# Kernel optimization log

Measured on AMD Instinct MI355X. Metric: run time of the kernel, lower is better.

## Reference

```python
import jax, jax.numpy as jnp
import numpy as np

NODE_DIM = 512
PROMPT_DIM = 512
N_NODES = 100000
N_GRAPHS = 1024


def setup_inputs() -> dict:
    key = jax.random.key(0)
    k1, k2, k3, k4, k5, k6, k7 = jax.random.split(key, 7)
    node_feats = jax.random.normal(k1, (N_NODES, NODE_DIM), dtype=jnp.float32)
    graph_prompt = jax.random.normal(k2, (N_GRAPHS, PROMPT_DIM), dtype=jnp.float32)
    batch_idx = jnp.sort(jax.random.randint(k3, (N_NODES,), 0, N_GRAPHS))
    # Linear init ~ U(-1/sqrt(fan_in), 1/sqrt(fan_in)) like torch defaults
    fan1 = NODE_DIM + PROMPT_DIM
    b1 = 1.0 / np.sqrt(fan1)
    W1 = jax.random.uniform(k4, (fan1, NODE_DIM), minval=-b1, maxval=b1, dtype=jnp.float32)
    bias1 = jax.random.uniform(k5, (NODE_DIM,), minval=-b1, maxval=b1, dtype=jnp.float32)
    b2 = 1.0 / np.sqrt(NODE_DIM)
    W2 = jax.random.uniform(k6, (NODE_DIM, NODE_DIM), minval=-b2, maxval=b2, dtype=jnp.float32)
    bias2 = jax.random.uniform(k7, (NODE_DIM,), minval=-b2, maxval=b2, dtype=jnp.float32)
    return {"node_feats": node_feats, "graph_prompt": graph_prompt, "batch_idx": batch_idx,
            "W1": W1, "bias1": bias1, "W2": W2, "bias2": bias2}


def reference(node_feats, graph_prompt, batch_idx, W1, bias1, W2, bias2):
    # gather per-node prompt: [N, prompt_dim]
    prompt_expanded = graph_prompt[batch_idx]
    combined = jnp.concatenate([node_feats, prompt_expanded], axis=-1)  # [N, node_dim+prompt_dim]
    h = jax.nn.relu(combined @ W1 + bias1)  # [N, node_dim]
    return h @ W2 + bias2  # [N, node_dim]
```

## Files before the change

### kernel.cpp

```cpp
#include <hip/hip_runtime.h>


#define N_NODES 100000
#define MT1 782
#define NWG (MT1 * 4)

typedef __bf16 bf16x8 __attribute__((ext_vector_type(8)));
typedef float  f32x4  __attribute__((ext_vector_type(4)));
typedef unsigned short ushort_t;

__device__ __forceinline__ ushort_t f2bf(float f) {
  __bf16 b = (__bf16)f;
  return __builtin_bit_cast(unsigned short, b);
}

__device__ __forceinline__ bf16x8 cvt8(const float* p) {
  float4 x = *(const float4*)p;
  float4 y = *(const float4*)(p + 4);
  bf16x8 v;
  v[0] = (__bf16)x.x; v[1] = (__bf16)x.y; v[2] = (__bf16)x.z; v[3] = (__bf16)x.w;
  v[4] = (__bf16)y.x; v[5] = (__bf16)y.y; v[6] = (__bf16)y.z; v[7] = (__bf16)y.w;
  return v;
}

__device__ __forceinline__ bf16x8 cvt8v(float4 x, float4 y) {
  bf16x8 v;
  v[0] = (__bf16)x.x; v[1] = (__bf16)x.y; v[2] = (__bf16)x.z; v[3] = (__bf16)x.w;
  v[4] = (__bf16)y.x; v[5] = (__bf16)y.y; v[6] = (__bf16)y.z; v[7] = (__bf16)y.w;
  return v;
}

__device__ __forceinline__ void gload_lds16(const void* g, void* l) {
  __builtin_amdgcn_global_load_lds(
      (const __attribute__((address_space(1))) void*)g,
      (__attribute__((address_space(3))) void*)l, 16, 0, 0);
}

__global__ void prep_kernel(const float* __restrict__ W1, const float* __restrict__ W2,
                            ushort_t* __restrict__ W1T, ushort_t* __restrict__ W2T) {
  int i = blockIdx.x * 256 + threadIdx.x;
  if (i < 524288) {
    int n = i >> 10, k = i & 1023;
    W1T[i] = f2bf(W1[k * 512 + n]);
  } else if (i < 786432) {
    int j = i - 524288;
    int n = j >> 9, k = j & 511;
    W2T[j] = f2bf(W2[k * 512 + n]);
  }
}

__global__ __launch_bounds__(256, 4) void p2_kernel(
    const float* __restrict__ gp, const ushort_t* __restrict__ W1T,
    const float* __restrict__ bias1, float* __restrict__ P2) {
  const int tid = threadIdx.x, lane = tid & 63, wid = tid >> 6;
  const int lc = lane & 15, lr = lane >> 4;
  const int m0 = (blockIdx.x >> 1) * 32;
  const int col0 = (blockIdx.x & 1) * 256 + wid * 64;

  f32x4 acc[2][4];
#pragma unroll
  for (int i = 0; i < 2; ++i)
#pragma unroll
    for (int j = 0; j < 4; ++j) acc[i][j] = {0.f, 0.f, 0.f, 0.f};

  const float* a0 = gp + (size_t)(m0 + lc) * 512;
  const ushort_t* bb = W1T + (size_t)(col0 + lc) * 1024 + 512;

#pragma unroll 2
  for (int kt = 0; kt < 8; ++kt) {
    bf16x8 bfr[2][4];
#pragma unroll
    for (int kk = 0; kk < 2; ++kk)
#pragma unroll
      for (int j = 0; j < 4; ++j)
        bfr[kk][j] = *(const bf16x8*)(bb + (size_t)j * 16 * 1024 + kt * 64 + kk * 32 + lr * 8);
    bf16x8 af[2][2];
#pragma unroll
    for (int i = 0; i < 2; ++i)
#pragma unroll
      for (int kk = 0; kk < 2; ++kk)
        af[i][kk] = cvt8(a0 + (size_t)i * 16 * 512 + kt * 64 + kk * 32 + lr * 8);
#pragma unroll
    for (int kk = 0; kk < 2; ++kk)
#pragma unroll
      for (int i = 0; i < 2; ++i)
#pragma unroll
        for (int j = 0; j < 4; ++j)
          acc[i][j] = __builtin_amdgcn_mfma_f32_16x16x32_bf16(af[i][kk], bfr[kk][j], acc[i][j], 0, 0, 0);
  }

#pragma unroll
  for (int i = 0; i < 2; ++i)
#pragma unroll
    for (int r = 0; r < 4; ++r) {
      int row = m0 + i * 16 + lr * 4 + r;
#pragma unroll
      for (int j = 0; j < 4; ++j) {
        int col = col0 + j * 16 + lc;
        P2[(size_t)row * 512 + col] = acc[i][j][r] + bias1[col];
      }
    }
}

__global__ __launch_bounds__(256, 3) void g1_kernel(
    const float* __restrict__ nf, const int* __restrict__ bidx,
    const ushort_t* __restrict__ W1T, const float* __restrict__ P2,
    ushort_t* __restrict__ h) {
  __shared__ float    sAf[128 * 64];
  __shared__ ushort_t sB[128 * 64];

  const int tid = threadIdx.x, lane = tid & 63, wid = tid >> 6;
  const int tile = (blockIdx.x & 7) * 391 + (blockIdx.x >> 3);
  const int m0 = (tile >> 2) * 128, n0 = (tile & 3) * 128;

  const float* pA[8]; int ldsA[8];
#pragma unroll
  for (int s = 0; s < 8; ++s) {
    int q = s * 256 + tid;
    int row = q >> 4;
    int cw = (q & 15) ^ (row & 15);
    int rowg = m0 + row; if (rowg > N_NODES - 1) rowg = N_NODES - 1;
    pA[s] = nf + (size_t)rowg * 512 + cw * 4;
    ldsA[s] = (s * 256 + wid * 64) * 4;
  }
  const ushort_t* pB[4]; int ldsB[4];
#pragma unroll
  for (int s = 0; s < 4; ++s) {
    int q = wid * 256 + s * 64 + lane;
    int row = q >> 3;
    int cw = (q & 7) ^ (row & 7);
    pB[s] = W1T + (size_t)(n0 + row) * 1024 + cw * 8;
    ldsB[s] = (wid * 256 + s * 64) * 8;
  }

  f32x4 acc[4][4];
#pragma unroll
  for (int i = 0; i < 4; ++i)
#pragma unroll
    for (int j = 0; j < 4; ++j) acc[i][j] = {0.f, 0.f, 0.f, 0.f};

  const int wm = (wid >> 1) * 64, wn = (wid & 1) * 64;
  const int lr = lane >> 4, lc = lane & 15;

  for (int kt = 0; kt < 8; ++kt) {
#pragma unroll
    for (int s = 0; s < 8; ++s) { gload_lds16(pA[s], &sAf[ldsA[s]]); pA[s] += 64; }
#pragma unroll
    for (int s = 0; s < 4; ++s) { gload_lds16(pB[s], &sB[ldsB[s]]); pB[s] += 64; }
    __syncthreads();

#pragma unroll
    for (int kk = 0; kk < 2; ++kk) {
      bf16x8 af[4], bfr[4];
#pragma unroll
      for (int i = 0; i < 4; ++i) {
        int row = wm + i * 16 + lc;
        int c0 = kk * 8 + lr * 2;
        int p0 = c0 ^ (row & 15);
        int p1 = (c0 + 1) ^ (row & 15);
        float4 x = *(const float4*)&sAf[row * 64 + p0 * 4];
        float4 y = *(const float4*)&sAf[row * 64 + p1 * 4];
        af[i] = cvt8v(x, y);
      }
#pragma unroll
      for (int j = 0; j < 4; ++j) {
        int col = wn + j * 16 + lc;
        int cp = (kk * 4 + lr) ^ (col & 7);
        bfr[j] = *(const bf16x8*)&sB[col * 64 + cp * 8];
      }
#pragma unroll
      for (int i = 0; i < 4; ++i)
#pragma unroll
        for (int j = 0; j < 4; ++j)
          acc[i][j] = __builtin_amdgcn_mfma_f32_16x16x32_bf16(af[i], bfr[j], acc[i][j], 0, 0, 0);
    }
    __syncthreads();
  }

#pragma unroll
  for (int i = 0; i < 4; ++i) {
#pragma unroll
    for (int r = 0; r < 4; ++r) {
      int row = m0 + wm + i * 16 + lr * 4 + r;
      if (row < N_NODES) {
        int g = bidx[row];
        const float* p2r = P2 + (size_t)g * 512 + n0 + wn;
#pragma unroll
        for (int j = 0; j < 4; ++j) {
          float v = fmaxf(acc[i][j][r] + p2r[j * 16 + lc], 0.f);
          h[(size_t)row * 512 + n0 + wn + j * 16 + lc] = f2bf(v);
        }
      }
    }
  }
}

__global__ __launch_bounds__(256, 4) void g2_kernel(
    const ushort_t* __restrict__ h, const ushort_t* __restrict__ W2T,
    const float* __restrict__ bias2, float* __restrict__ out) {
  __shared__ ushort_t sA[128 * 64];
  __shared__ ushort_t sB[128 * 64];

  const int tid = threadIdx.x, lane = tid & 63, wid = tid >> 6;
  const int tile = (blockIdx.x & 7) * 391 + (blockIdx.x >> 3);
  const int m0 = (tile >> 2) * 128, n0 = (tile & 3) * 128;

  const ushort_t* pA[4]; const ushort_t* pB[4]; int ldsW[4];
#pragma unroll
  for (int s = 0; s < 4; ++s) {
    int q = wid * 256 + s * 64 + lane;
    int row = q >> 3;
    int cw = (q & 7) ^ (row & 7);
    int rowg = m0 + row; if (rowg > N_NODES - 1) rowg = N_NODES - 1;
    pA[s] = h + (size_t)rowg * 512 + cw * 8;
    pB[s] = W2T + (size_t)(n0 + row) * 512 + cw * 8;
    ldsW[s] = (wid * 256 + s * 64) * 8;
  }

  f32x4 acc[4][4];
#pragma unroll
  for (int i = 0; i < 4; ++i)
#pragma unroll
    for (int j = 0; j < 4; ++j) acc[i][j] = {0.f, 0.f, 0.f, 0.f};

  const int wm = (wid >> 1) * 64, wn = (wid & 1) * 64;
  const int lr = lane >> 4, lc = lane & 15;

  for (int kt = 0; kt < 8; ++kt) {
#pragma unroll
    for (int s = 0; s < 4; ++s) {
      gload_lds16(pA[s], &sA[ldsW[s]]); pA[s] += 64;
      gload_lds16(pB[s], &sB[ldsW[s]]); pB[s] += 64;
    }
    __syncthreads();
#pragma unroll
    for (int kk = 0; kk < 2; ++kk) {
      bf16x8 af[4], bfr[4];
#pragma unroll
      for (int i = 0; i < 4; ++i) {
        int row = wm + i * 16 + lc;
        int cp = (kk * 4 + lr) ^ (row & 7);
        af[i] = *(const bf16x8*)&sA[row * 64 + cp * 8];
      }
#pragma unroll
      for (int j = 0; j < 4; ++j) {
        int col = wn + j * 16 + lc;
        int cp = (kk * 4 + lr) ^ (col & 7);
        bfr[j] = *(const bf16x8*)&sB[col * 64 + cp * 8];
      }
#pragma unroll
      for (int i = 0; i < 4; ++i)
#pragma unroll
        for (int j = 0; j < 4; ++j)
          acc[i][j] = __builtin_amdgcn_mfma_f32_16x16x32_bf16(af[i], bfr[j], acc[i][j], 0, 0, 0);
    }
    __syncthreads();
  }

#pragma unroll
  for (int j = 0; j < 4; ++j) {
    int col = n0 + wn + j * 16 + lc;
    float bv = bias2[col];
#pragma unroll
    for (int i = 0; i < 4; ++i)
#pragma unroll
      for (int r = 0; r < 4; ++r) {
        int row = m0 + wm + i * 16 + lr * 4 + r;
        if (row < N_NODES) out[(size_t)row * 512 + col] = acc[i][j][r] + bv;
      }
  }
}

extern "C" void kernel_launch(void* const* d_in, const int* in_sizes, int n_in,
                              void* d_out, int out_size, void* d_ws, size_t ws_size,
                              hipStream_t stream) {
  const float* nf   = (const float*)d_in[0];
  const float* gp   = (const float*)d_in[1];
  const int*   bidx = (const int*)d_in[2];
  const float* W1   = (const float*)d_in[3];
  const float* b1   = (const float*)d_in[4];
  const float* W2   = (const float*)d_in[5];
  const float* b2   = (const float*)d_in[6];
  float* out = (float*)d_out;

  char* ws = (char*)d_ws;
  ushort_t* W1T = (ushort_t*)ws;
  ushort_t* W2T = (ushort_t*)(ws + 1048576);
  float*    P2  = (float*)   (ws + 1572864);
  ushort_t* hbf = (ushort_t*)(ws + 3670016);

  prep_kernel<<<3072, 256, 0, stream>>>(W1, W2, W1T, W2T);
  p2_kernel<<<64, 256, 0, stream>>>(gp, W1T, b1, P2);
  g1_kernel<<<NWG, 256, 0, stream>>>(nf, bidx, W1T, P2, hbf);
  g2_kernel<<<NWG, 256, 0, stream>>>(hbf, W2T, b2, out);
}
```

Baseline: 295.2 us.

## Double-buffer LDS tiles with K=32 steps in both GEMM kernels

Both GEMM kernels now split the K loop into 16 steps of 32 instead of 8 steps of 64. They keep two LDS buffers and issue the global-to-LDS loads for step k+1 before the MFMA work of step k, which removes one barrier per iteration. The goal is to overlap memory latency with compute at the same LDS footprint. In exchange the swizzle is narrower (4- or 8-way XOR), which may raise LDS bank conflicts, and each synchronized step does less work.

Result: slower. 312.2 us (+5.7%).

```diff
diff --git a/kernel.cpp b/kernel.cpp
--- a/kernel.cpp
+++ b/kernel.cpp
@@ -2,8 +2,7 @@
 
 
 #define N_NODES 100000
-#define MT1 782
-#define NWG (MT1 * 4)
+#define NWG 3128
 
 typedef __bf16 bf16x8 __attribute__((ext_vector_type(8)));
 typedef float  f32x4  __attribute__((ext_vector_type(4)));
@@ -106,31 +105,31 @@
     const float* __restrict__ nf, const int* __restrict__ bidx,
     const ushort_t* __restrict__ W1T, const float* __restrict__ P2,
     ushort_t* __restrict__ h) {
-  __shared__ float    sAf[128 * 64];
-  __shared__ ushort_t sB[128 * 64];
+  __shared__ float    sAf[2][128 * 32];
+  __shared__ ushort_t sB[2][128 * 32];
 
   const int tid = threadIdx.x, lane = tid & 63, wid = tid >> 6;
   const int tile = (blockIdx.x & 7) * 391 + (blockIdx.x >> 3);
   const int m0 = (tile >> 2) * 128, n0 = (tile & 3) * 128;
 
-  const float* pA[8]; int ldsA[8];
-#pragma unroll
-  for (int s = 0; s < 8; ++s) {
+  const float* pA[4]; int ldsA[4];
+#pragma unroll
+  for (int s = 0; s < 4; ++s) {
     int q = s * 256 + tid;
-    int row = q >> 4;
-    int cw = (q & 15) ^ (row & 15);
+    int row = q >> 3;
+    int cw = (q & 7) ^ (row & 7);
     int rowg = m0 + row; if (rowg > N_NODES - 1) rowg = N_NODES - 1;
     pA[s] = nf + (size_t)rowg * 512 + cw * 4;
     ldsA[s] = (s * 256 + wid * 64) * 4;
   }
-  const ushort_t* pB[4]; int ldsB[4];
-#pragma unroll
-  for (int s = 0; s < 4; ++s) {
-    int q = wid * 256 + s * 64 + lane;
-    int row = q >> 3;
-    int cw = (q & 7) ^ (row & 7);
+  const ushort_t* pB[2]; int ldsB[2];
+#pragma unroll
+  for (int s = 0; s < 2; ++s) {
+    int q = s * 256 + tid;
+    int row = q >> 2;
+    int cw = (q & 3) ^ (row & 3);
     pB[s] = W1T + (size_t)(n0 + row) * 1024 + cw * 8;
-    ldsB[s] = (wid * 256 + s * 64) * 8;
+    ldsB[s] = (s * 256 + wid * 64) * 8;
   }
 
   f32x4 acc[4][4];
@@ -142,39 +141,43 @@
   const int wm = (wid >> 1) * 64, wn = (wid & 1) * 64;
   const int lr = lane >> 4, lc = lane & 15;
 
-  for (int kt = 0; kt < 8; ++kt) {
-#pragma unroll
-    for (int s = 0; s < 8; ++s) { gload_lds16(pA[s], &sAf[ldsA[s]]); pA[s] += 64; }
-#pragma unroll
-    for (int s = 0; s < 4; ++s) { gload_lds16(pB[s], &sB[ldsB[s]]); pB[s] += 64; }
-    __syncthreads();
-
-#pragma unroll
-    for (int kk = 0; kk < 2; ++kk) {
-      bf16x8 af[4], bfr[4];
-#pragma unroll
-      for (int i = 0; i < 4; ++i) {
-        int row = wm + i * 16 + lc;
-        int c0 = kk * 8 + lr * 2;
-        int p0 = c0 ^ (row & 15);
-        int p1 = (c0 + 1) ^ (row & 15);
-        float4 x = *(const float4*)&sAf[row * 64 + p0 * 4];
-        float4 y = *(const float4*)&sAf[row * 64 + p1 * 4];
-        af[i] = cvt8v(x, y);
-      }
-#pragma unroll
-      for (int j = 0; j < 4; ++j) {
-        int col = wn + j * 16 + lc;
-        int cp = (kk * 4 + lr) ^ (col & 7);
-        bfr[j] = *(const bf16x8*)&sB[col * 64 + cp * 8];
-      }
-#pragma unroll
-      for (int i = 0; i < 4; ++i)
-#pragma unroll
-        for (int j = 0; j < 4; ++j)
-          acc[i][j] = __builtin_amdgcn_mfma_f32_16x16x32_bf16(af[i], bfr[j], acc[i][j], 0, 0, 0);
-    }
-    __syncthreads();
+#pragma unroll
+  for (int s = 0; s < 4; ++s) { gload_lds16(pA[s], &sAf[0][ldsA[s]]); pA[s] += 32; }
+#pragma unroll
+  for (int s = 0; s < 2; ++s) { gload_lds16(pB[s], &sB[0][ldsB[s]]); pB[s] += 32; }
+  __syncthreads();
+
+#pragma unroll
+  for (int kt = 0; kt < 16; ++kt) {
+    const int cur = kt & 1;
+    if (kt < 15) {
+#pragma unroll
+      for (int s = 0; s < 4; ++s) { gload_lds16(pA[s], &sAf[cur ^ 1][ldsA[s]]); pA[s] += 32; }
+#pragma unroll
+      for (int s = 0; s < 2; ++s) { gload_lds16(pB[s], &sB[cur ^ 1][ldsB[s]]); pB[s] += 32; }
+    }
+    bf16x8 af[4], bfr[4];
+#pragma unroll
+    for (int i = 0; i < 4; ++i) {
+      int row = wm + i * 16 + lc;
+      int p0 = (lr * 2) ^ (row & 7);
+      int p1 = (lr * 2 + 1) ^ (row & 7);
+      float4 x = *(const float4*)&sAf[cur][row * 32 + p0 * 4];
+      float4 y = *(const float4*)&sAf[cur][row * 32 + p1 * 4];
+      af[i] = cvt8v(x, y);
+    }
+#pragma unroll
+    for (int j = 0; j < 4; ++j) {
+      int col = wn + j * 16 + lc;
+      int pb = lr ^ (col & 3);
+      bfr[j] = *(const bf16x8*)&sB[cur][col * 32 + pb * 8];
+    }
+#pragma unroll
+    for (int i = 0; i < 4; ++i)
+#pragma unroll
+      for (int j = 0; j < 4; ++j)
+        acc[i][j] = __builtin_amdgcn_mfma_f32_16x16x32_bf16(af[i], bfr[j], acc[i][j], 0, 0, 0);
+    if (kt < 15) __syncthreads();
   }
 
 #pragma unroll
@@ -198,23 +201,23 @@
 __global__ __launch_bounds__(256, 4) void g2_kernel(
     const ushort_t* __restrict__ h, const ushort_t* __restrict__ W2T,
     const float* __restrict__ bias2, float* __restrict__ out) {
-  __shared__ ushort_t sA[128 * 64];
-  __shared__ ushort_t sB[128 * 64];
+  __shared__ ushort_t sA[2][128 * 32];
+  __shared__ ushort_t sB[2][128 * 32];
 
   const int tid = threadIdx.x, lane = tid & 63, wid = tid >> 6;
   const int tile = (blockIdx.x & 7) * 391 + (blockIdx.x >> 3);
   const int m0 = (tile >> 2) * 128, n0 = (tile & 3) * 128;
 
-  const ushort_t* pA[4]; const ushort_t* pB[4]; int ldsW[4];
-#pragma unroll
-  for (int s = 0; s < 4; ++s) {
-    int q = wid * 256 + s * 64 + lane;
-    int row = q >> 3;
-    int cw = (q & 7) ^ (row & 7);
+  const ushort_t* pA[2]; const ushort_t* pB[2]; int ldsW[2];
+#pragma unroll
+  for (int s = 0; s < 2; ++s) {
+    int q = s * 256 + tid;
+    int row = q >> 2;
+    int cw = (q & 3) ^ (row & 3);
     int rowg = m0 + row; if (rowg > N_NODES - 1) rowg = N_NODES - 1;
     pA[s] = h + (size_t)rowg * 512 + cw * 8;
     pB[s] = W2T + (size_t)(n0 + row) * 512 + cw * 8;
-    ldsW[s] = (wid * 256 + s * 64) * 8;
+    ldsW[s] = (s * 256 + wid * 64) * 8;
   }
 
   f32x4 acc[4][4];
@@ -226,35 +229,42 @@
   const int wm = (wid >> 1) * 64, wn = (wid & 1) * 64;
   const int lr = lane >> 4, lc = lane & 15;
 
-  for (int kt = 0; kt < 8; ++kt) {
-#pragma unroll
-    for (int s = 0; s < 4; ++s) {
-      gload_lds16(pA[s], &sA[ldsW[s]]); pA[s] += 64;
-      gload_lds16(pB[s], &sB[ldsW[s]]); pB[s] += 64;
-    }
-    __syncthreads();
-#pragma unroll
-    for (int kk = 0; kk < 2; ++kk) {
-      bf16x8 af[4], bfr[4];
-#pragma unroll
-      for (int i = 0; i < 4; ++i) {
-        int row = wm + i * 16 + lc;
-        int cp = (kk * 4 + lr) ^ (row & 7);
-        af[i] = *(const bf16x8*)&sA[row * 64 + cp * 8];
+#pragma unroll
+  for (int s = 0; s < 2; ++s) {
+    gload_lds16(pA[s], &sA[0][ldsW[s]]); pA[s] += 32;
+    gload_lds16(pB[s], &sB[0][ldsW[s]]); pB[s] += 32;
+  }
+  __syncthreads();
+
+#pragma unroll
+  for (int kt = 0; kt < 16; ++kt) {
+    const int cur = kt & 1;
+    if (kt < 15) {
+#pragma unroll
+      for (int s = 0; s < 2; ++s) {
+        gload_lds16(pA[s], &sA[cur ^ 1][ldsW[s]]); pA[s] += 32;
+        gload_lds16(pB[s], &sB[cur ^ 1][ldsW[s]]); pB[s] += 32;
       }
-#pragma unroll
-      for (int j = 0; j < 4; ++j) {
-        int col = wn + j * 16 + lc;
-        int cp = (kk * 4 + lr) ^ (col & 7);
-        bfr[j] = *(const bf16x8*)&sB[col * 64 + cp * 8];
-      }
-#pragma unroll
-      for (int i = 0; i < 4; ++i)
-#pragma unroll
-        for (int j = 0; j < 4; ++j)
-          acc[i][j] = __builtin_amdgcn_mfma_f32_16x16x32_bf16(af[i], bfr[j], acc[i][j], 0, 0, 0);
-    }
-    __syncthreads();
+    }
+    bf16x8 af[4], bfr[4];
+#pragma unroll
+    for (int i = 0; i < 4; ++i) {
+      int row = wm + i * 16 + lc;
+      int pa = lr ^ (row & 3);
+      af[i] = *(const bf16x8*)&sA[cur][row * 32 + pa * 8];
+    }
+#pragma unroll
+    for (int j = 0; j < 4; ++j) {
+      int col = wn + j * 16 + lc;
+      int pb = lr ^ (col & 3);
+      bfr[j] = *(const bf16x8*)&sB[cur][col * 32 + pb * 8];
+    }
+#pragma unroll
+    for (int i = 0; i < 4; ++i)
+#pragma unroll
+      for (int j = 0; j < 4; ++j)
+        acc[i][j] = __builtin_amdgcn_mfma_f32_16x16x32_bf16(af[i], bfr[j], acc[i][j], 0, 0, 0);
+    if (kt < 15) __syncthreads();
   }
 
 #pragma unroll
```
